# Kernel tuning notes

Hardware: AMD Instinct MI355X
Metric: run time of the kernel (lower is better)

## Reference

```python
import jax, jax.numpy as jnp
import numpy as np

N_NODES = 50000
N_EDGES = 800000
IN_CH = 128
HEADS = 4
OUT_CH = 32


def setup_inputs() -> dict:
    key = jax.random.key(0)
    k1, k2, k3, k4 = jax.random.split(key, 4)
    x = jax.random.normal(k1, (N_NODES, IN_CH), dtype=jnp.float32)
    edge_index = jax.random.randint(k2, (2, N_EDGES), 0, N_NODES, dtype=jnp.int64)
    # nn.Linear weight [out, in] with xavier-uniform init
    limW = float(np.sqrt(6.0 / (IN_CH + HEADS * OUT_CH)))
    W = jax.random.uniform(k3, (HEADS * OUT_CH, IN_CH), minval=-limW, maxval=limW, dtype=jnp.float32)
    lima = float(np.sqrt(6.0 / (HEADS + 2 * OUT_CH)))
    att = jax.random.uniform(k4, (HEADS, 2 * OUT_CH), minval=-lima, maxval=lima, dtype=jnp.float32)
    bias = jnp.zeros((HEADS * OUT_CH,), dtype=jnp.float32)
    return {"x": x, "edge_index": edge_index, "W": W, "att": att, "bias": bias}


def reference(x, edge_index, W, att, bias):
    n = x.shape[0]
    heads, two_c = att.shape
    out_ch = two_c // 2
    loop = jnp.arange(n, dtype=edge_index.dtype)
    src = jnp.concatenate([edge_index[0], loop])  # [E+n]
    dst = jnp.concatenate([edge_index[1], loop])  # [E+n]
    h = (x @ W.T).reshape(n, heads, out_ch)       # [n, H, C]
    h_src = h[src]                                # [E+n, H, C]
    h_dst = h[dst]                                # [E+n, H, C]
    # e = sum over channels of att applied to [h_src || h_dst]
    e = (jnp.einsum('ehc,hc->eh', h_src, att[:, :out_ch])
         + jnp.einsum('ehc,hc->eh', h_dst, att[:, out_ch:]))  # [E+n, H]
    e = jax.nn.leaky_relu(e, negative_slope=0.2)
    # segment softmax over incoming edges per dst node
    e_max = jax.ops.segment_max(e, dst, num_segments=n)        # [n, H]
    alpha = jnp.exp(e - e_max[dst])                            # [E+n, H]
    a_sum = jax.ops.segment_sum(alpha, dst, num_segments=n)    # [n, H]
    alpha = alpha / jnp.maximum(a_sum[dst], 1e-10)
    weighted = h_src * alpha[..., None]                        # [E+n, H, C]
    out = jax.ops.segment_sum(weighted, dst, num_segments=n)   # [n, H, C]
    out = out.reshape(n, heads * out_ch)                       # concat=True
    return out + bias
```

## Files before the change

### kernel.cpp

```cpp
#include <hip/hip_runtime.h>
#include <hip/hip_bf16.h>
#include <math.h>

#define N_NODES 50000
#define N_EDGES 800000
#define IN_CH   128
#define HEADS   4
#define OUT_CH  32
#define HC      128
#define WROWS   136

#define CB_SHIFT 5
#define CB_NODES 32
#define N_CB     1563
#define NBK      128
#define EPB      (N_EDGES / NBK)
#define PCAP     20
#define ND_CAP   48

#define NG_TOT   391

typedef __attribute__((ext_vector_type(8))) short short8;
typedef __attribute__((ext_vector_type(8))) unsigned short ushort8;
typedef __attribute__((ext_vector_type(4))) float floatx4;

__device__ __forceinline__ short f2bf(float f) {
    __hip_bfloat16 h = __float2bfloat16(f);
    return *reinterpret_cast<short*>(&h);
}

__device__ __forceinline__ void gemm_role(
    short* __restrict__ Wlds, int node_base,
    const float* __restrict__ x, const float* __restrict__ W,
    const float* __restrict__ att, __hip_bfloat16* __restrict__ hbuf,
    float* __restrict__ asrc, float* __restrict__ adst) {

    const int tid  = threadIdx.x;
    const int wave = tid >> 6;
    const int lane = tid & 63;
    const int col  = lane & 15;
    const int q    = lane >> 4;

    {
        int row  = tid >> 2;
        int quar = tid & 3;
        const float4* Wr = (const float4*)(W + row * IN_CH + quar * 32);
        short* dp = Wlds + row * WROWS + quar * 32;
#pragma unroll
        for (int i = 0; i < 8; ++i) {
            float4 v = Wr[i];
            ushort4 p;
            p.x = (unsigned short)f2bf(v.x);
            p.y = (unsigned short)f2bf(v.y);
            p.z = (unsigned short)f2bf(v.z);
            p.w = (unsigned short)f2bf(v.w);
            *(ushort4*)(dp + i * 4) = p;
        }
    }

    float attS[8], attD[8];
#pragma unroll
    for (int t = 0; t < 8; ++t) {
        int base = (t >> 1) * 64 + (t & 1) * 16 + col;
        attS[t] = att[base];
        attD[t] = att[base + 32];
    }

    __syncthreads();

    const int node0 = node_base + wave * 16;
    const int m  = node0 + col;
    const int mc = min(m, N_NODES - 1);

    floatx4 acc[8];
#pragma unroll
    for (int t = 0; t < 8; ++t) acc[t] = (floatx4){0.f, 0.f, 0.f, 0.f};

#pragma unroll
    for (int ks = 0; ks < 4; ++ks) {
        const float4* xp = (const float4*)(x + (size_t)mc * IN_CH + ks * 32 + q * 8);
        float4 v0 = xp[0];
        float4 v1 = xp[1];
        short8 af;
        af[0] = f2bf(v0.x); af[1] = f2bf(v0.y); af[2] = f2bf(v0.z); af[3] = f2bf(v0.w);
        af[4] = f2bf(v1.x); af[5] = f2bf(v1.y); af[6] = f2bf(v1.z); af[7] = f2bf(v1.w);
#pragma unroll
        for (int t = 0; t < 8; ++t) {
            const short8 bf = *(const short8*)(Wlds + (t * 16 + col) * WROWS + ks * 32 + q * 8);
            acc[t] = __builtin_amdgcn_mfma_f32_16x16x32_bf16(af, bf, acc[t], 0, 0, 0);
        }
    }

#pragma unroll
    for (int r = 0; r < 4; ++r) {
        const int node = node0 + q * 4 + r;
        const bool valid = node < N_NODES;
        float hs[4] = {0.f, 0.f, 0.f, 0.f};
        float hd[4] = {0.f, 0.f, 0.f, 0.f};
#pragma unroll
        for (int t = 0; t < 8; ++t) {
            float v = acc[t][r];
            if (valid) hbuf[(size_t)node * HC + t * 16 + col] = __float2bfloat16(v);
            hs[t >> 1] = fmaf(v, attS[t], hs[t >> 1]);
            hd[t >> 1] = fmaf(v, attD[t], hd[t >> 1]);
        }
#pragma unroll
        for (int off = 8; off; off >>= 1) {
#pragma unroll
            for (int h = 0; h < 4; ++h) {
                hs[h] += __shfl_down(hs[h], off, 16);
                hd[h] += __shfl_down(hd[h], off, 16);
            }
        }
        if (col == 0 && valid) {
#pragma unroll
            for (int h = 0; h < 4; ++h) {
                asrc[node * HEADS + h] = hs[h];
                adst[node * HEADS + h] = hd[h];
            }
        }
    }
}

__global__ __launch_bounds__(512, 4) void k1_fused(
    const int* __restrict__ src, const int* __restrict__ dst,
    unsigned* __restrict__ priv, int* __restrict__ cnt2t,
    const float* __restrict__ x, const float* __restrict__ W,
    const float* __restrict__ att, __hip_bfloat16* __restrict__ hbuf,
    float* __restrict__ asrc, float* __restrict__ adst) {

    __shared__ short smem[128 * WROWS];
    const int tid = threadIdx.x;

    if (blockIdx.x < NBK) {
        int* lcnt = (int*)smem;
        const int blk = blockIdx.x;
        for (int i = tid; i < N_CB; i += 512) lcnt[i] = 0;
        __syncthreads();

        const int e0 = blk * EPB;
        for (int e = e0 + tid; e < e0 + EPB; e += 512) {
            int s = src[e];
            int d = dst[e];
            int cb = d >> CB_SHIFT;
            int pos = atomicAdd(&lcnt[cb], 1);
            if (pos < PCAP)
                priv[((size_t)cb * NBK + blk) * PCAP + pos] =
                    ((unsigned)(d & (CB_NODES - 1)) << 16) | (unsigned)s;
        }
        __syncthreads();
        for (int i = tid; i < N_CB; i += 512)
            cnt2t[i * NBK + blk] = min(lcnt[i], PCAP);
        return;
    }

    gemm_role(smem, (blockIdx.x - NBK) * 128, x, W, att, hbuf, asrc, adst);
}

__device__ __forceinline__ float edge_w(float t) {
    t = fmaxf(t, 0.2f * t);
    return __expf(t);
}

__device__ __forceinline__ void agg_one(
    int node, int cnt, const unsigned short* __restrict__ p,
    const unsigned* __restrict__ hb, const float* __restrict__ asrc,
    const float* __restrict__ adst, float2 bv,
    float* __restrict__ out, int lane, int h) {

    const float ad = adst[node * HEADS + h];

    unsigned us = hb[node * 64 + lane];
    float wS = edge_w(asrc[node * HEADS + h] + ad);
    float ds = wS;
    float ax = wS * __uint_as_float(us << 16);
    float ay = wS * __uint_as_float(us & 0xffff0000u);

    int e = 0;
    for (; e + 7 < cnt; e += 8) {
        ushort8 sv = *(const ushort8*)(p + e);
        int s0 = sv[0], s1 = sv[1], s2 = sv[2], s3 = sv[3];
        int s4 = sv[4], s5 = sv[5], s6 = sv[6], s7 = sv[7];
        unsigned u0 = hb[s0 * 64 + lane];
        unsigned u1 = hb[s1 * 64 + lane];
        unsigned u2 = hb[s2 * 64 + lane];
        unsigned u3 = hb[s3 * 64 + lane];
        unsigned u4 = hb[s4 * 64 + lane];
        unsigned u5 = hb[s5 * 64 + lane];
        unsigned u6 = hb[s6 * 64 + lane];
        unsigned u7 = hb[s7 * 64 + lane];
        float w0 = edge_w(asrc[s0 * HEADS + h] + ad);
        float w1 = edge_w(asrc[s1 * HEADS + h] + ad);
        float w2 = edge_w(asrc[s2 * HEADS + h] + ad);
        float w3 = edge_w(asrc[s3 * HEADS + h] + ad);
        float w4 = edge_w(asrc[s4 * HEADS + h] + ad);
        float w5 = edge_w(asrc[s5 * HEADS + h] + ad);
        float w6 = edge_w(asrc[s6 * HEADS + h] + ad);
        float w7 = edge_w(asrc[s7 * HEADS + h] + ad);
        ds += ((w0 + w1) + (w2 + w3)) + ((w4 + w5) + (w6 + w7));
        ax = fmaf(w0, __uint_as_float(u0 << 16), ax);
        ay = fmaf(w0, __uint_as_float(u0 & 0xffff0000u), ay);
        ax = fmaf(w1, __uint_as_float(u1 << 16), ax);
        ay = fmaf(w1, __uint_as_float(u1 & 0xffff0000u), ay);
        ax = fmaf(w2, __uint_as_float(u2 << 16), ax);
        ay = fmaf(w2, __uint_as_float(u2 & 0xffff0000u), ay);
        ax = fmaf(w3, __uint_as_float(u3 << 16), ax);
        ay = fmaf(w3, __uint_as_float(u3 & 0xffff0000u), ay);
        ax = fmaf(w4, __uint_as_float(u4 << 16), ax);
        ay = fmaf(w4, __uint_as_float(u4 & 0xffff0000u), ay);
        ax = fmaf(w5, __uint_as_float(u5 << 16), ax);
        ay = fmaf(w5, __uint_as_float(u5 & 0xffff0000u), ay);
        ax = fmaf(w6, __uint_as_float(u6 << 16), ax);
        ay = fmaf(w6, __uint_as_float(u6 & 0xffff0000u), ay);
        ax = fmaf(w7, __uint_as_float(u7 << 16), ax);
        ay = fmaf(w7, __uint_as_float(u7 & 0xffff0000u), ay);
    }
    for (; e + 3 < cnt; e += 4) {
        int s0 = p[e], s1 = p[e + 1], s2 = p[e + 2], s3 = p[e + 3];
        unsigned u0 = hb[s0 * 64 + lane];
        unsigned u1 = hb[s1 * 64 + lane];
        unsigned u2 = hb[s2 * 64 + lane];
        unsigned u3 = hb[s3 * 64 + lane];
        float w0 = edge_w(asrc[s0 * HEADS + h] + ad);
        float w1 = edge_w(asrc[s1 * HEADS + h] + ad);
        float w2 = edge_w(asrc[s2 * HEADS + h] + ad);
        float w3 = edge_w(asrc[s3 * HEADS + h] + ad);
        ds += (w0 + w1) + (w2 + w3);
        ax = fmaf(w0, __uint_as_float(u0 << 16), ax);
        ay = fmaf(w0, __uint_as_float(u0 & 0xffff0000u), ay);
        ax = fmaf(w1, __uint_as_float(u1 << 16), ax);
        ay = fmaf(w1, __uint_as_float(u1 & 0xffff0000u), ay);
        ax = fmaf(w2, __uint_as_float(u2 << 16), ax);
        ay = fmaf(w2, __uint_as_float(u2 & 0xffff0000u), ay);
        ax = fmaf(w3, __uint_as_float(u3 << 16), ax);
        ay = fmaf(w3, __uint_as_float(u3 & 0xffff0000u), ay);
    }
    for (; e < cnt; ++e) {
        int s0 = p[e];
        unsigned u0 = hb[s0 * 64 + lane];
        float w0 = edge_w(asrc[s0 * HEADS + h] + ad);
        ds += w0;
        ax = fmaf(w0, __uint_as_float(u0 << 16), ax);
        ay = fmaf(w0, __uint_as_float(u0 & 0xffff0000u), ay);
    }

    float inv = 1.0f / fmaxf(ds, 1e-10f);
    float2 o;
    o.x = ax * inv + bv.x;
    o.y = ay * inv + bv.y;
    *(float2*)(out + (size_t)node * HC + lane * 2) = o;
}

__global__ __launch_bounds__(512) void k2_binagg(
    const int* __restrict__ cnt2t, const unsigned* __restrict__ priv,
    const unsigned* __restrict__ hb, const float* __restrict__ asrc,
    const float* __restrict__ adst, const float* __restrict__ bias,
    float* __restrict__ out) {

    __shared__ unsigned short list[CB_NODES * ND_CAP];
    __shared__ int lcnt[CB_NODES];
    __shared__ int lcnt2[NBK];

    const int b   = blockIdx.x;
    const int tid = threadIdx.x;

    if (tid < CB_NODES) lcnt[tid] = 0;
    if (tid < NBK) lcnt2[tid] = cnt2t[b * NBK + tid];
    __syncthreads();

    const unsigned* p = priv + (size_t)b * (NBK * PCAP);
    for (int idx = tid; idx < NBK * PCAP; idx += 512) {
        int blk = (idx * 3277) >> 16;
        int j   = idx - blk * PCAP;
        if (j < lcnt2[blk]) {
            unsigned ent = p[idx];
            int dl   = ent >> 16;
            int slot = atomicAdd(&lcnt[dl], 1);
            if (slot < ND_CAP)
                list[dl * ND_CAP + slot] = (unsigned short)(ent & 0xFFFFu);
        }
    }
    __syncthreads();

    const int wv   = tid >> 6;
    const int lane = tid & 63;
    const int h    = lane >> 4;
    const float2 bv = *(const float2*)(bias + lane * 2);

#pragma unroll 1
    for (int rr = 0; rr < 4; ++rr) {
        const int dl   = (wv << 2) + rr;
        const int node = (b << CB_SHIFT) + dl;
        if (node >= N_NODES) break;
        const int cnt = min(lcnt[dl], ND_CAP);
        agg_one(node, cnt, &list[dl * ND_CAP],
                hb, asrc, adst, bv, out, lane, h);
    }
}

extern "C" void kernel_launch(void* const* d_in, const int* in_sizes, int n_in,
                              void* d_out, int out_size, void* d_ws, size_t ws_size,
                              hipStream_t stream) {
    const float* x    = (const float*)d_in[0];
    const int*   ei   = (const int*)d_in[1];
    const float* W    = (const float*)d_in[2];
    const float* att  = (const float*)d_in[3];
    const float* bias = (const float*)d_in[4];
    float* out = (float*)d_out;

    const int* src = ei;
    const int* dst = ei + N_EDGES;

    char* ws = (char*)d_ws;
    __hip_bfloat16* hbuf = (__hip_bfloat16*)ws;
    float*    asrc = (float*)(ws + 12800000);
    float*    adst = (float*)(ws + 13600000);
    unsigned* priv = (unsigned*)(ws + 14400000);
    int*      cnt2 = (int*)(ws + 30405120);

    k1_fused<<<NBK + NG_TOT, 512, 0, stream>>>(src, dst, priv, cnt2,
                                               x, W, att, hbuf, asrc, adst);
    k2_binagg<<<N_CB, 512, 0, stream>>>(cnt2, priv, (const unsigned*)hbuf,
                                        asrc, adst, bias, out);
}
```

Before: 140.3 us.

## Replace fixed-capacity per-block edge bins with densely packed counting-sort buckets

The edge-binning blocks now run two passes. They first count edges per destination chunk, then take a block-wide prefix scan and scatter the packed entries into a dense per-block buffer in shared memory, writing it out coalesced along with start/count metadata. The aggregation kernel reads only the valid entries through this metadata instead of scanning a padded 20-slot-per-chunk array, which cuts global writes and reads of mostly empty slots. In exchange the edge list is read twice, the per-chunk counter is clamped to 255, and shared memory per block grows.

```diff
diff --git a/kernel.cpp b/kernel.cpp
--- a/kernel.cpp
+++ b/kernel.cpp
@@ -15,10 +15,11 @@
 #define N_CB     1563
 #define NBK      128
 #define EPB      (N_EDGES / NBK)
-#define PCAP     20
 #define ND_CAP   48
 
 #define NG_TOT   391
+
+#define SMEM_BYTES 37568
 
 typedef __attribute__((ext_vector_type(8))) short short8;
 typedef __attribute__((ext_vector_type(8))) unsigned short ushort8;
@@ -124,37 +125,80 @@
 
 __global__ __launch_bounds__(512, 4) void k1_fused(
     const int* __restrict__ src, const int* __restrict__ dst,
-    unsigned* __restrict__ priv, int* __restrict__ cnt2t,
+    unsigned* __restrict__ dense, unsigned* __restrict__ meta,
     const float* __restrict__ x, const float* __restrict__ W,
     const float* __restrict__ att, __hip_bfloat16* __restrict__ hbuf,
     float* __restrict__ asrc, float* __restrict__ adst) {
 
-    __shared__ short smem[128 * WROWS];
+    __shared__ char smem[SMEM_BYTES];
     const int tid = threadIdx.x;
 
     if (blockIdx.x < NBK) {
-        int* lcnt = (int*)smem;
+        int*      lcnt   = (int*)smem;
+        int*      lstart = (int*)(smem + 6252);
+        unsigned* outb   = (unsigned*)(smem + 12504);
+        int*      wps    = (int*)(smem + 37504);
+
         const int blk = blockIdx.x;
+        const int e0  = blk * EPB;
+
         for (int i = tid; i < N_CB; i += 512) lcnt[i] = 0;
         __syncthreads();
 
-        const int e0 = blk * EPB;
+        for (int e = e0 + tid; e < e0 + EPB; e += 512)
+            atomicAdd(&lcnt[dst[e] >> CB_SHIFT], 1);
+        __syncthreads();
+
+        const int base = tid * 4;
+        int s0 = 0, s1 = 0, s2 = 0, s3 = 0;
+        if (base < N_CB) {
+            s0 = lcnt[base];
+            s1 = (base + 1 < N_CB) ? lcnt[base + 1] : 0;
+            s2 = (base + 2 < N_CB) ? lcnt[base + 2] : 0;
+            s3 = (base + 3 < N_CB) ? lcnt[base + 3] : 0;
+        }
+        const int tsum = s0 + s1 + s2 + s3;
+        const int lane = tid & 63;
+        int incl = tsum;
+#pragma unroll
+        for (int off = 1; off < 64; off <<= 1) {
+            int v = __shfl_up(incl, off, 64);
+            if (lane >= off) incl += v;
+        }
+        if (lane == 63) wps[tid >> 6] = incl;
+        __syncthreads();
+        int wexcl = 0;
+        const int wv = tid >> 6;
+#pragma unroll
+        for (int w = 0; w < 8; ++w) if (w < wv) wexcl += wps[w];
+        const int excl = wexcl + incl - tsum;
+        if (base < N_CB) {
+            lstart[base] = excl;
+            if (base + 1 < N_CB) lstart[base + 1] = excl + s0;
+            if (base + 2 < N_CB) lstart[base + 2] = excl + s0 + s1;
+            if (base + 3 < N_CB) lstart[base + 3] = excl + s0 + s1 + s2;
+        }
+        __syncthreads();
+
+        for (int i = tid; i < N_CB; i += 512)
+            meta[(size_t)blk * N_CB + i] =
+                ((unsigned)lstart[i] << 8) | (unsigned)min(lcnt[i], 255);
+        __syncthreads();
+
         for (int e = e0 + tid; e < e0 + EPB; e += 512) {
             int s = src[e];
             int d = dst[e];
-            int cb = d >> CB_SHIFT;
-            int pos = atomicAdd(&lcnt[cb], 1);
-            if (pos < PCAP)
-                priv[((size_t)cb * NBK + blk) * PCAP + pos] =
-                    ((unsigned)(d & (CB_NODES - 1)) << 16) | (unsigned)s;
-        }
-        __syncthreads();
-        for (int i = tid; i < N_CB; i += 512)
-            cnt2t[i * NBK + blk] = min(lcnt[i], PCAP);
+            int pos = atomicAdd(&lstart[d >> CB_SHIFT], 1);
+            outb[pos] = ((unsigned)(d & (CB_NODES - 1)) << 16) | (unsigned)s;
+        }
+        __syncthreads();
+
+        for (int i = tid; i < EPB; i += 512)
+            dense[(size_t)blk * EPB + i] = outb[i];
         return;
     }
 
-    gemm_role(smem, (blockIdx.x - NBK) * 128, x, W, att, hbuf, asrc, adst);
+    gemm_role((short*)smem, (blockIdx.x - NBK) * 128, x, W, att, hbuf, asrc, adst);
 }
 
 __device__ __forceinline__ float edge_w(float t) {
@@ -252,28 +296,29 @@
 }
 
 __global__ __launch_bounds__(512) void k2_binagg(
-    const int* __restrict__ cnt2t, const unsigned* __restrict__ priv,
+    const unsigned* __restrict__ meta, const unsigned* __restrict__ dense,
     const unsigned* __restrict__ hb, const float* __restrict__ asrc,
     const float* __restrict__ adst, const float* __restrict__ bias,
     float* __restrict__ out) {
 
     __shared__ unsigned short list[CB_NODES * ND_CAP];
     __shared__ int lcnt[CB_NODES];
-    __shared__ int lcnt2[NBK];
 
     const int b   = blockIdx.x;
     const int tid = threadIdx.x;
 
     if (tid < CB_NODES) lcnt[tid] = 0;
-    if (tid < NBK) lcnt2[tid] = cnt2t[b * NBK + tid];
     __syncthreads();
 
-    const unsigned* p = priv + (size_t)b * (NBK * PCAP);
-    for (int idx = tid; idx < NBK * PCAP; idx += 512) {
-        int blk = (idx * 3277) >> 16;
-        int j   = idx - blk * PCAP;
-        if (j < lcnt2[blk]) {
-            unsigned ent = p[idx];
+    {
+        const int blk = tid >> 2;
+        const int j0  = tid & 3;
+        unsigned mv = meta[(size_t)blk * N_CB + b];
+        int start = (int)(mv >> 8);
+        int cnt   = (int)(mv & 0xFFu);
+        const unsigned* pd = dense + (size_t)blk * EPB + start;
+        for (int j = j0; j < cnt; j += 4) {
+            unsigned ent = pd[j];
             int dl   = ent >> 16;
             int slot = atomicAdd(&lcnt[dl], 1);
             if (slot < ND_CAP)
@@ -313,13 +358,13 @@
 
     char* ws = (char*)d_ws;
     __hip_bfloat16* hbuf = (__hip_bfloat16*)ws;
-    float*    asrc = (float*)(ws + 12800000);
-    float*    adst = (float*)(ws + 13600000);
-    unsigned* priv = (unsigned*)(ws + 14400000);
-    int*      cnt2 = (int*)(ws + 30405120);
-
-    k1_fused<<<NBK + NG_TOT, 512, 0, stream>>>(src, dst, priv, cnt2,
+    float*    asrc  = (float*)(ws + 12800000);
+    float*    adst  = (float*)(ws + 13600000);
+    unsigned* dense = (unsigned*)(ws + 14400000);
+    unsigned* meta  = (unsigned*)(ws + 17600000);
+
+    k1_fused<<<NBK + NG_TOT, 512, 0, stream>>>(src, dst, dense, meta,
                                                x, W, att, hbuf, asrc, adst);
-    k2_binagg<<<N_CB, 512, 0, stream>>>(cnt2, priv, (const unsigned*)hbuf,
+    k2_binagg<<<N_CB, 512, 0, stream>>>(meta, dense, (const unsigned*)hbuf,
                                         asrc, adst, bias, out);
 }
```

Measured after the change: 137.0 us, median of 2. -2.4%, faster.
